# Optimization experiments

Hardware: AMD Instinct MI355X
Metric: run time of the kernel (lower is better)

The kernel has to match this reference:

```python
import jax, jax.numpy as jnp
import numpy as np

K = 7        # kernel_size
DIL = 2      # dilation (hardcoded in module)
PAD = 6      # padding, keeps spatial dims with stride=1
G = 8        # groups (group_channels = 16)


def setup_inputs() -> dict:
    key = jax.random.key(0)
    ks = jax.random.split(key, 5)
    B, C, H, W = 4, 128, 64, 64
    Cr = C // 4                      # red_ratio = 4
    KKG = K * K * G                  # 392
    return {
        "x": jax.random.normal(ks[0], (B, C, H, W), jnp.float32),
        "w_reduce": jax.random.normal(ks[1], (Cr, C), jnp.float32) * 0.05,
        "b_reduce": jax.random.normal(ks[2], (Cr,), jnp.float32) * 0.05,
        "w_span": jax.random.normal(ks[3], (KKG, Cr), jnp.float32) * 0.05,
        "b_span": jax.random.normal(ks[4], (KKG,), jnp.float32) * 0.05,
    }


def reference(x, w_reduce, b_reduce, w_span, b_span):
    B, C, H, W = x.shape
    Cg = C // G
    # kernel generation: two 1x1 convs (pointwise matmuls over channel dim)
    red = jnp.einsum('bchw,oc->bohw', x, w_reduce) + b_reduce[None, :, None, None]
    ker = jnp.einsum('bohw,ko->bkhw', red, w_span) + b_span[None, :, None, None]
    ker = ker.reshape(B, G, K * K, H, W)          # [B, G, KK, H, W]
    # unfold: dilated KxK patches, stride 1, 'same' output size
    xp = jnp.pad(x, ((0, 0), (0, 0), (PAD, PAD), (PAD, PAD)))
    patches = jnp.stack(
        [xp[:, :, i * DIL:i * DIL + H, j * DIL:j * DIL + W]
         for i in range(K) for j in range(K)], axis=2)  # [B, C, KK, H, W]
    patches = patches.reshape(B, G, Cg, K * K, H, W)
    # per-pixel dynamic kernel multiply + sum over window
    out = jnp.einsum('bgckhw,bgkhw->bgchw', patches, ker)
    return out.reshape(B, C, H, W)
```

## Files before the change

### kernel.cpp

```cpp
#include <hip/hip_runtime.h>


#define HW 4096
#define NC 128
#define NR 32
#define KK 49
#define KSTR 136

typedef __attribute__((ext_vector_type(8))) short short8;
typedef __attribute__((ext_vector_type(4))) float f32x4;

__device__ __forceinline__ unsigned short f2bf(float f) {
  unsigned int u = __float_as_uint(f);
  u = (u + 0x7fffu + ((u >> 16) & 1u)) >> 16;
  return (unsigned short)u;
}

__global__ __launch_bounds__(256) void red_gen(
    const float* __restrict__ x, const float* __restrict__ w_reduce,
    const float* __restrict__ b_reduce, unsigned short* __restrict__ red_bf) {
  __shared__ float xs[NC][64];
  int t = threadIdx.x;
  int blk = blockIdx.x;
  int b = blk >> 7;
  int sub = blk & 127;
  int row = sub >> 1;
  int oh = sub & 1;
  int p0 = row * 64;

  const float* xb = x + b * NC * HW + p0;
  int fx = t & 15;
  int c0 = t >> 4;
#pragma unroll
  for (int r = 0; r < 8; ++r) {
    int c = c0 + 16 * r;
    *(float4*)(&xs[c][fx * 4]) = *(const float4*)(xb + c * HW + fx * 4);
  }
  __syncthreads();

  int px = t & 63;
  int wv = __builtin_amdgcn_readfirstlane(t >> 6);
  int ob = oh * 16 + wv * 4;
  const float* wq = w_reduce + ob * NC;

  float acc[4];
#pragma unroll
  for (int j = 0; j < 4; ++j) acc[j] = b_reduce[ob + j];

#pragma unroll 8
  for (int k = 0; k < NC; ++k) {
    float xk = xs[k][px];
#pragma unroll
    for (int j = 0; j < 4; ++j) acc[j] += xk * wq[j * NC + k];
  }

  union { unsigned long long v; unsigned short u[4]; } pk;
#pragma unroll
  for (int j = 0; j < 4; ++j) pk.u[j] = f2bf(acc[j]);
  *(unsigned long long*)(red_bf + ((size_t)(b * HW) + p0 + px) * NR + ob) = pk.v;
}

__global__ __launch_bounds__(256) void inv_fused(
    const float* __restrict__ x, const unsigned short* __restrict__ red_bf,
    const float* __restrict__ w_span, const float* __restrict__ b_span,
    float* __restrict__ out) {
  __shared__ float kvs[KK * KSTR];
  __shared__ short wlds[64 * NR];
  __shared__ float bsl[64];

  int orig = blockIdx.x;
  int blk = (orig & 7) * 128 + (orig >> 3);
  int hp = blk & 31;
  int g = (blk >> 5) & 7;
  int b = blk >> 8;
  int tid = threadIdx.x;
  int h0 = hp * 2;
  int p0 = h0 * 64;

  const float* wg = w_span + g * KK * NR;
#pragma unroll
  for (int it = 0; it < 8; ++it) {
    int idx = it * 256 + tid;
    wlds[idx] = (idx < KK * NR) ? (short)f2bf(wg[idx]) : (short)0;
  }
  if (tid < 64) bsl[tid] = (tid < KK) ? b_span[g * KK + tid] : 0.f;
  __syncthreads();

  int l = tid & 63;
  int wv = __builtin_amdgcn_readfirstlane(tid >> 6);
  int quad = l >> 4;
  int mn = l & 15;

  short8 af[4];
#pragma unroll
  for (int tt = 0; tt < 4; ++tt)
    af[tt] = *(const short8*)(&wlds[(tt * 16 + mn) * NR + quad * 8]);

  f32x4 ci[4];
#pragma unroll
  for (int tt = 0; tt < 4; ++tt) {
#pragma unroll
    for (int r = 0; r < 4; ++r) ci[tt][r] = bsl[tt * 16 + quad * 4 + r];
  }

  const unsigned short* rb =
      red_bf + ((size_t)b * HW + p0 + wv * 32 + mn) * NR + quad * 8;
#pragma unroll
  for (int nt = 0; nt < 2; ++nt) {
    short8 bf = *(const short8*)(rb + (size_t)nt * 16 * NR);
    f32x4 d0 = __builtin_amdgcn_mfma_f32_16x16x32_bf16(af[0], bf, ci[0], 0, 0, 0);
    f32x4 d1 = __builtin_amdgcn_mfma_f32_16x16x32_bf16(af[1], bf, ci[1], 0, 0, 0);
    f32x4 d2 = __builtin_amdgcn_mfma_f32_16x16x32_bf16(af[2], bf, ci[2], 0, 0, 0);
    f32x4 d3 = __builtin_amdgcn_mfma_f32_16x16x32_bf16(af[3], bf, ci[3], 0, 0, 0);
    int pxl = wv * 32 + nt * 16 + mn;
    int r = pxl >> 6, col = pxl & 63;
    float* dst = &kvs[r * 68 + col];
#pragma unroll
    for (int rg = 0; rg < 4; ++rg) {
      dst[(size_t)(0 * 16 + quad * 4 + rg) * KSTR] = d0[rg];
      dst[(size_t)(1 * 16 + quad * 4 + rg) * KSTR] = d1[rg];
      dst[(size_t)(2 * 16 + quad * 4 + rg) * KSTR] = d2[rg];
    }
    if (quad == 0) dst[(size_t)48 * KSTR] = d3[0];
  }
  __syncthreads();

  int c = tid >> 4;
  int sub = tid & 15;
  int r = sub >> 3;
  int oct = sub & 7;

  const float* xc = x + ((size_t)(b * NC + g * 16 + c)) * HW + 8 * oct - 8;
  int mo0 = 0, mo1 = 4, mo4 = 16, mo5 = 20;
  if (oct == 0) { mo0 = 8; mo1 = 12; }
  if (oct == 7) { mo4 = 8; mo5 = 12; }

  float2 a0 = {0.f, 0.f}, a1 = {0.f, 0.f}, a2 = {0.f, 0.f}, a3 = {0.f, 0.f};

#pragma unroll
  for (int i = 0; i < 7; ++i) {
    int rbase = h0 + 2 * i - 6;
    if (rbase < 0 || rbase > 62) continue;
    const float* pr = xc + (size_t)(rbase + r) * 64;
    float xr[24];
    float4 v;
    v = *(const float4*)(pr + mo0); xr[0]=v.x; xr[1]=v.y; xr[2]=v.z; xr[3]=v.w;
    v = *(const float4*)(pr + mo1); xr[4]=v.x; xr[5]=v.y; xr[6]=v.z; xr[7]=v.w;
    v = *(const float4*)(pr + 8);   xr[8]=v.x; xr[9]=v.y; xr[10]=v.z; xr[11]=v.w;
    v = *(const float4*)(pr + 12);  xr[12]=v.x; xr[13]=v.y; xr[14]=v.z; xr[15]=v.w;
    v = *(const float4*)(pr + mo4); xr[16]=v.x; xr[17]=v.y; xr[18]=v.z; xr[19]=v.w;
    v = *(const float4*)(pr + mo5); xr[20]=v.x; xr[21]=v.y; xr[22]=v.z; xr[23]=v.w;
    if (oct == 0) { xr[2]=0.f; xr[3]=0.f; xr[4]=0.f; xr[5]=0.f; xr[6]=0.f; xr[7]=0.f; }
    if (oct == 7) { xr[16]=0.f; xr[17]=0.f; xr[18]=0.f; xr[19]=0.f; xr[20]=0.f; xr[21]=0.f; }
#pragma unroll
    for (int j = 0; j < 7; ++j) {
      const float* kb = &kvs[(i * 7 + j) * KSTR + r * 68 + 8 * oct];
      float4 k0 = *(const float4*)(kb);
      float4 k1 = *(const float4*)(kb + 4);
      a0.x = fmaf(xr[2 + 2 * j], k0.x, a0.x);
      a0.y = fmaf(xr[3 + 2 * j], k0.y, a0.y);
      a1.x = fmaf(xr[4 + 2 * j], k0.z, a1.x);
      a1.y = fmaf(xr[5 + 2 * j], k0.w, a1.y);
      a2.x = fmaf(xr[6 + 2 * j], k1.x, a2.x);
      a2.y = fmaf(xr[7 + 2 * j], k1.y, a2.y);
      a3.x = fmaf(xr[8 + 2 * j], k1.z, a3.x);
      a3.y = fmaf(xr[9 + 2 * j], k1.w, a3.y);
    }
  }

  int h = h0 + r;
  float* op = out + (size_t)(b * NC + g * 16 + c) * HW + h * 64 + 8 * oct;
  *(float4*)op = make_float4(a0.x, a0.y, a1.x, a1.y);
  *(float4*)(op + 4) = make_float4(a2.x, a2.y, a3.x, a3.y);
}

extern "C" void kernel_launch(void* const* d_in, const int* in_sizes, int n_in,
                              void* d_out, int out_size, void* d_ws, size_t ws_size,
                              hipStream_t stream) {
  const float* x        = (const float*)d_in[0];
  const float* w_reduce = (const float*)d_in[1];
  const float* b_reduce = (const float*)d_in[2];
  const float* w_span   = (const float*)d_in[3];
  const float* b_span   = (const float*)d_in[4];
  float* out = (float*)d_out;

  unsigned short* red_bf = (unsigned short*)d_ws;

  red_gen<<<512, 256, 0, stream>>>(x, w_reduce, b_reduce, red_bf);
  inv_fused<<<1024, 256, 0, stream>>>(x, red_bf, w_span, b_span, out);
}
```

Measured before the change: 85.33 us.

## Fuse channel-reduce conv into the involution kernel, removing the separate launch

```diff
diff --git a/kernel.cpp b/kernel.cpp
--- a/kernel.cpp
+++ b/kernel.cpp
@@ -16,57 +16,14 @@
   return (unsigned short)u;
 }
 
-__global__ __launch_bounds__(256) void red_gen(
+__global__ __launch_bounds__(256) void inv_one(
     const float* __restrict__ x, const float* __restrict__ w_reduce,
-    const float* __restrict__ b_reduce, unsigned short* __restrict__ red_bf) {
-  __shared__ float xs[NC][64];
-  int t = threadIdx.x;
-  int blk = blockIdx.x;
-  int b = blk >> 7;
-  int sub = blk & 127;
-  int row = sub >> 1;
-  int oh = sub & 1;
-  int p0 = row * 64;
-
-  const float* xb = x + b * NC * HW + p0;
-  int fx = t & 15;
-  int c0 = t >> 4;
-#pragma unroll
-  for (int r = 0; r < 8; ++r) {
-    int c = c0 + 16 * r;
-    *(float4*)(&xs[c][fx * 4]) = *(const float4*)(xb + c * HW + fx * 4);
-  }
-  __syncthreads();
-
-  int px = t & 63;
-  int wv = __builtin_amdgcn_readfirstlane(t >> 6);
-  int ob = oh * 16 + wv * 4;
-  const float* wq = w_reduce + ob * NC;
-
-  float acc[4];
-#pragma unroll
-  for (int j = 0; j < 4; ++j) acc[j] = b_reduce[ob + j];
-
-#pragma unroll 8
-  for (int k = 0; k < NC; ++k) {
-    float xk = xs[k][px];
-#pragma unroll
-    for (int j = 0; j < 4; ++j) acc[j] += xk * wq[j * NC + k];
-  }
-
-  union { unsigned long long v; unsigned short u[4]; } pk;
-#pragma unroll
-  for (int j = 0; j < 4; ++j) pk.u[j] = f2bf(acc[j]);
-  *(unsigned long long*)(red_bf + ((size_t)(b * HW) + p0 + px) * NR + ob) = pk.v;
-}
-
-__global__ __launch_bounds__(256) void inv_fused(
-    const float* __restrict__ x, const unsigned short* __restrict__ red_bf,
-    const float* __restrict__ w_span, const float* __restrict__ b_span,
-    float* __restrict__ out) {
+    const float* __restrict__ b_reduce, const float* __restrict__ w_span,
+    const float* __restrict__ b_span, float* __restrict__ out) {
   __shared__ float kvs[KK * KSTR];
   __shared__ short wlds[64 * NR];
   __shared__ float bsl[64];
+  __shared__ unsigned short redl[128 * NR];
 
   int orig = blockIdx.x;
   int blk = (orig & 7) * 128 + (orig >> 3);
@@ -84,12 +41,36 @@
     wlds[idx] = (idx < KK * NR) ? (short)f2bf(wg[idx]) : (short)0;
   }
   if (tid < 64) bsl[tid] = (tid < KK) ? b_span[g * KK + tid] : 0.f;
-  __syncthreads();
 
   int l = tid & 63;
   int wv = __builtin_amdgcn_readfirstlane(tid >> 6);
   int quad = l >> 4;
   int mn = l & 15;
+
+  {
+    int ob = (wv >> 1) * 16;
+    int pl = (wv & 1) * 64 + l;
+    const float* wq = w_reduce + ob * NC;
+    const float* xpx = x + (size_t)b * NC * HW + p0 + pl;
+
+    float acc[16];
+#pragma unroll
+    for (int j = 0; j < 16; ++j) acc[j] = b_reduce[ob + j];
+
+#pragma unroll 4
+    for (int k = 0; k < NC; ++k) {
+      float xk = xpx[(size_t)k * HW];
+#pragma unroll
+      for (int j = 0; j < 16; ++j) acc[j] = fmaf(xk, wq[j * NC + k], acc[j]);
+    }
+
+    union { short8 v; unsigned short u[8]; } pk0, pk1;
+#pragma unroll
+    for (int j = 0; j < 8; ++j) { pk0.u[j] = f2bf(acc[j]); pk1.u[j] = f2bf(acc[8 + j]); }
+    *(short8*)(&redl[pl * NR + ob]) = pk0.v;
+    *(short8*)(&redl[pl * NR + ob + 8]) = pk1.v;
+  }
+  __syncthreads();
 
   short8 af[4];
 #pragma unroll
@@ -103,11 +84,10 @@
     for (int r = 0; r < 4; ++r) ci[tt][r] = bsl[tt * 16 + quad * 4 + r];
   }
 
-  const unsigned short* rb =
-      red_bf + ((size_t)b * HW + p0 + wv * 32 + mn) * NR + quad * 8;
+  const unsigned short* rl = &redl[(wv * 32 + mn) * NR + quad * 8];
 #pragma unroll
   for (int nt = 0; nt < 2; ++nt) {
-    short8 bf = *(const short8*)(rb + (size_t)nt * 16 * NR);
+    short8 bf = *(const short8*)(rl + nt * 16 * NR);
     f32x4 d0 = __builtin_amdgcn_mfma_f32_16x16x32_bf16(af[0], bf, ci[0], 0, 0, 0);
     f32x4 d1 = __builtin_amdgcn_mfma_f32_16x16x32_bf16(af[1], bf, ci[1], 0, 0, 0);
     f32x4 d2 = __builtin_amdgcn_mfma_f32_16x16x32_bf16(af[2], bf, ci[2], 0, 0, 0);
@@ -184,8 +164,5 @@
   const float* b_span   = (const float*)d_in[4];
   float* out = (float*)d_out;
 
-  unsigned short* red_bf = (unsigned short*)d_ws;
-
-  red_gen<<<512, 256, 0, stream>>>(x, w_reduce, b_reduce, red_bf);
-  inv_fused<<<1024, 256, 0, stream>>>(x, red_bf, w_span, b_span, out);
+  inv_one<<<1024, 256, 0, stream>>>(x, w_reduce, b_reduce, w_span, b_span, out);
 }
```

Result: slower. 93.79 us (+9.9%).
